# Kernel tuning notes

Hardware: AMD Instinct MI355X
Metric: run time of the kernel (lower is better)

The kernel has to match this reference:

```python
import jax, jax.numpy as jnp
import numpy as np

B, S, D = 2, 2048, 2048
H, HKV, HD = 16, 2, 128
THETA = 10000.0


def setup_inputs() -> dict:
    key = jax.random.key(0)
    ks = jax.random.split(key, 5)
    x = jax.random.normal(ks[0], (B, S, D), jnp.float32)
    Wq = jax.random.normal(ks[1], (D, H * HD), jnp.float32) * 0.02
    Wk = jax.random.normal(ks[2], (D, HKV * HD), jnp.float32) * 0.02
    Wv = jax.random.normal(ks[3], (D, HKV * HD), jnp.float32) * 0.02
    Wo = jax.random.normal(ks[4], (H * HD, D), jnp.float32) * 0.02
    mask = jnp.tril(jnp.ones((S, S), jnp.int32))[None, None]  # causal [1,1,S,S]
    return {"x": x, "mask": mask, "Wq": Wq, "Wk": Wk, "Wv": Wv, "Wo": Wo}


def _rope(t, seq_len):
    # t: [B, S, H, HD]; matches RotaryPositionalEmbedding (cos/sin broadcast [S,1,HD])
    inv_freq = 1.0 / (THETA ** (jnp.arange(0, HD, 2, dtype=jnp.float32) / HD))
    pos = jnp.arange(seq_len, dtype=jnp.float32)
    freqs = jnp.einsum('i,j->ij', pos, inv_freq)          # [S, HD/2]
    emb = jnp.concatenate([freqs, freqs], axis=-1)        # [S, HD]
    cos = jnp.cos(emb)[:, None, :]
    sin = jnp.sin(emb)[:, None, :]
    x1, x2 = jnp.split(t, 2, axis=-1)
    rot = jnp.concatenate([-x2, x1], axis=-1)             # rotate_half
    return t * cos + rot * sin


def reference(x, mask, Wq, Wk, Wv, Wo):
    Bx, Sx, _ = x.shape
    q = (x @ Wq).reshape(Bx, Sx, H, HD)
    k = (x @ Wk).reshape(Bx, Sx, HKV, HD)
    v = (x @ Wv).reshape(Bx, Sx, HKV, HD)
    q = _rope(q, Sx)
    k = _rope(k, Sx)
    rep = H // HKV
    # torch .repeat along head dim == tiling (not interleaved)
    k = jnp.tile(k, (1, 1, rep, 1))  # [B, S, H, HD]
    v = jnp.tile(v, (1, 1, rep, 1))
    scale = 1.0 / np.sqrt(HD).astype(np.float32)
    scores = jnp.einsum('bqhd,bkhd->bhqk', q, k) * scale  # [B, H, S, S]
    scores = jnp.where(mask == 0, -jnp.inf, scores)
    attn = jax.nn.softmax(scores.astype(jnp.float32), axis=-1).astype(scores.dtype)
    out = jnp.einsum('bhqk,bkhd->bqhd', attn, v).reshape(Bx, Sx, H * HD)
    return out @ Wo
```

## Files before the change

### kernel.cpp

```cpp
#include <hip/hip_runtime.h>
#include <hip/hip_bf16.h>

#define S_LEN 2048
#define DMODEL 2048
#define NHEAD 16
#define NKVH 2
#define HDIM 128
#define NROW 4096
#define NQKV 2560
#define SCALE 0.08838834764831845f
#define LOG2E 1.4426950408889634f

using short8 = __attribute__((ext_vector_type(8))) short;
using bf16x8 = __attribute__((ext_vector_type(8))) __bf16;
using f32x4  = __attribute__((ext_vector_type(4))) float;

__device__ __forceinline__ f32x4 mfma16(short8 a, short8 b, f32x4 c) {
  return __builtin_amdgcn_mfma_f32_16x16x32_bf16(
      __builtin_bit_cast(bf16x8, a), __builtin_bit_cast(bf16x8, b), c, 0, 0, 0);
}

__device__ __forceinline__ void gload_lds16(const void* g, void* l) {
  __builtin_amdgcn_global_load_lds(
      (const __attribute__((address_space(1))) unsigned int*)g,
      (__attribute__((address_space(3))) unsigned int*)l, 16, 0, 0);
}

__device__ __forceinline__ float fast_exp2(float x) {
  return __builtin_amdgcn_exp2f(x);
}

__device__ __forceinline__ void storeC(float* C, long idx, float v) { C[idx] = v; }
__device__ __forceinline__ void storeC(__hip_bfloat16* C, long idx, float v) {
  C[idx] = __float2bfloat16(v);
}

__device__ __forceinline__ unsigned short bf16bits(float f) {
  __hip_bfloat16 h = __float2bfloat16(f);
  return *(unsigned short*)&h;
}

__global__ void prep_kernel(const float* __restrict__ x, __hip_bfloat16* __restrict__ xb,
                            const float* __restrict__ Wq, const float* __restrict__ Wk,
                            const float* __restrict__ Wv, __hip_bfloat16* __restrict__ wt1,
                            const float* __restrict__ Wo, __hip_bfloat16* __restrict__ wto,
                            float* __restrict__ cost, float* __restrict__ sint) {
  __shared__ float t[32][33];
  const int bid = blockIdx.x;
  const int tid = threadIdx.x;
  if (bid < 8192) {
    long i = ((long)bid * 256 + tid) * 4;
    float4 v = *(const float4*)(x + i);
    __hip_bfloat16 o[4];
    o[0] = __float2bfloat16(v.x); o[1] = __float2bfloat16(v.y);
    o[2] = __float2bfloat16(v.z); o[3] = __float2bfloat16(v.w);
    *(ushort4*)(xb + i) = *(const ushort4*)o;
  } else if (bid < 17408) {
    int tx = tid & 31, ty = tid >> 5;
    const float* src; int Ns, n0, row_off, kt;
    __hip_bfloat16* dst;
    if (bid < 13312) {
      int r = bid - 8192;
      int nt = r % 80; kt = r / 80;
      dst = wt1;
      if (nt < 64)      { src = Wq; Ns = 2048; n0 = nt * 32;        row_off = n0; }
      else if (nt < 72) { src = Wk; Ns = 256;  n0 = (nt - 64) * 32; row_off = 2048 + n0; }
      else              { src = Wv; Ns = 256;  n0 = (nt - 72) * 32; row_off = 2304 + n0; }
    } else {
      int r = bid - 13312;
      int nt = r % 64; kt = r / 64;
      src = Wo; Ns = 2048; n0 = nt * 32; row_off = n0;
      dst = wto;
    }
#pragma unroll
    for (int i = 0; i < 4; i++)
      t[ty + i * 8][tx] = src[(long)(kt * 32 + ty + i * 8) * Ns + n0 + tx];
    __syncthreads();
#pragma unroll
    for (int i = 0; i < 4; i++)
      dst[(long)(row_off + ty + i * 8) * 2048 + kt * 32 + tx] =
          __float2bfloat16(t[tx][ty + i * 8]);
  } else {
    int i = (bid - 17408) * 256 + tid;
    int s = i >> 6, j = i & 63;
    float f = powf(10000.0f, -(float)j / 64.0f);
    float a = (float)s * f;
    cost[i] = cosf(a);
    sint[i] = sinf(a);
  }
}

template <typename OutT>
__global__ void gemm_bt(const __hip_bfloat16* __restrict__ A,
                        const __hip_bfloat16* __restrict__ Bt,
                        OutT* __restrict__ C, int M, int N, int K) {
  __shared__ __align__(16) __hip_bfloat16 a_lds[2][128 * 32];
  __shared__ __align__(16) __hip_bfloat16 b_lds[2][128 * 32];
  const int tid = threadIdx.x;
  const int wid = tid >> 6, lane = tid & 63;
  const int nbx = gridDim.x;
  int bid = blockIdx.y * nbx + blockIdx.x;
  const int nwg = nbx * gridDim.y;
  bid = (bid & 7) * (nwg >> 3) + (bid >> 3);
  const int m0 = (bid / nbx) * 128, n0 = (bid % nbx) * 128;
  const int wr = wid >> 1, wc = wid & 1;
  const int lrow = lane & 15, lk = lane >> 4;

  const __hip_bfloat16* ag0 = A + (long)(m0 + wid * 16 + (lane >> 2)) * K + (lane & 3) * 8;
  const __hip_bfloat16* bg0 = Bt + (long)(n0 + wid * 16 + (lane >> 2)) * K + (lane & 3) * 8;
  char* al0 = (char*)&a_lds[0][0] + wid * 1024 + lane * 16;
  char* al1 = (char*)&a_lds[1][0] + wid * 1024 + lane * 16;
  char* bl0 = (char*)&b_lds[0][0] + wid * 1024 + lane * 16;
  char* bl1 = (char*)&b_lds[1][0] + wid * 1024 + lane * 16;

  f32x4 acc[4][4] = {};

  for (int k0 = 0; k0 < K; k0 += 64) {
    gload_lds16(ag0 + k0, al0);
    gload_lds16(ag0 + 64 * (long)K + k0, al0 + 4096);
    gload_lds16(ag0 + k0 + 32, al1);
    gload_lds16(ag0 + 64 * (long)K + k0 + 32, al1 + 4096);
    gload_lds16(bg0 + k0, bl0);
    gload_lds16(bg0 + 64 * (long)K + k0, bl0 + 4096);
    gload_lds16(bg0 + k0 + 32, bl1);
    gload_lds16(bg0 + 64 * (long)K + k0 + 32, bl1 + 4096);
    __syncthreads();
#pragma unroll
    for (int hh = 0; hh < 2; hh++) {
      short8 af[4], bfr[4];
#pragma unroll
      for (int mi = 0; mi < 4; mi++)
        af[mi] = *(const short8*)(&a_lds[hh][0] + (wr * 64 + mi * 16 + lrow) * 32 + lk * 8);
#pragma unroll
      for (int ni = 0; ni < 4; ni++)
        bfr[ni] = *(const short8*)(&b_lds[hh][0] + (wc * 64 + ni * 16 + lrow) * 32 + lk * 8);
#pragma unroll
      for (int mi = 0; mi < 4; mi++)
#pragma unroll
        for (int ni = 0; ni < 4; ni++)
          acc[mi][ni] = mfma16(af[mi], bfr[ni], acc[mi][ni]);
    }
    __syncthreads();
  }
#pragma unroll
  for (int mi = 0; mi < 4; mi++)
#pragma unroll
    for (int ni = 0; ni < 4; ni++)
#pragma unroll
      for (int r = 0; r < 4; r++) {
        long row = m0 + wr * 64 + mi * 16 + lk * 4 + r;
        long col = n0 + wc * 64 + ni * 16 + lrow;
        storeC(C, row * N + col, acc[mi][ni][r]);
      }
}

__global__ void rope_vtrans(const __hip_bfloat16* __restrict__ qkv,
                            const float* __restrict__ cost, const float* __restrict__ sint,
                            __hip_bfloat16* __restrict__ q_r, __hip_bfloat16* __restrict__ k_t,
                            __hip_bfloat16* __restrict__ v_t) {
  __shared__ __hip_bfloat16 t[32][33];
  const int bid = blockIdx.x;
  const int tid = threadIdx.x;
  if (bid < 18432) {
    long row = (long)bid * 4 + (tid >> 6);
    int j = tid & 63;
    int hh = (int)(row % 18);
    long bs = row / 18;
    int s = (int)(bs & (S_LEN - 1));
    int b = (int)(bs >> 11);
    const __hip_bfloat16* src = qkv + bs * NQKV;
    float c = cost[s * 64 + j], sn = sint[s * 64 + j];
    if (hh < NHEAD) {
      int col0 = hh * HDIM;
      float lo = __bfloat162float(src[col0 + j]);
      float hi = __bfloat162float(src[col0 + j + 64]);
      __hip_bfloat16* dst = q_r + ((long)(b * NHEAD + hh) * S_LEN + s) * HDIM;
      const float qs = SCALE * LOG2E;
      dst[j]      = __float2bfloat16((lo * c - hi * sn) * qs);
      dst[j + 64] = __float2bfloat16((hi * c + lo * sn) * qs);
    } else {
      int kvh = hh - NHEAD;
      int col0 = DMODEL + kvh * HDIM;
      float lo = __bfloat162float(src[col0 + j]);
      float hi = __bfloat162float(src[col0 + j + 64]);
      long tb = (long)(b * NKVH + kvh) * (S_LEN * HDIM) + (long)(s >> 5) * 4096 +
                (s & 15) * 8 + (j & 7);
      int cs4 = ((s >> 4) & 1) * 4;
      int lkq = ((j >> 3) & 3) * 16;
      int dch = j >> 5;
      k_t[tb + (long)((cs4 + dch) * 64 + lkq) * 8]     = __float2bfloat16(lo * c - hi * sn);
      k_t[tb + (long)((cs4 + dch + 2) * 64 + lkq) * 8] = __float2bfloat16(hi * c + lo * sn);
    }
  } else {
    int r = bid - 18432;
    int st = r & 63, dt = (r >> 6) & 3, bk = r >> 8;
    int tx = tid & 31, ty = tid >> 5;
#pragma unroll
    for (int i = 0; i < 4; i++)
      t[ty + i * 8][tx] = qkv[((long)(bk >> 1) * S_LEN + st * 32 + ty + i * 8) * NQKV +
                              DMODEL + NKVH * HDIM + (bk & 1) * HDIM + dt * 32 + tx];
    __syncthreads();
    long base = (long)bk * (S_LEN * HDIM) + (long)st * 4096 + (tx >> 3) * 128 + (tx & 7);
#pragma unroll
    for (int i = 0; i < 4; i++) {
      int d = dt * 32 + ty + i * 8;
      v_t[base + (long)((d >> 4) * 64 + (d & 15)) * 8] = t[tx][ty + i * 8];
    }
  }
}

__global__ __launch_bounds__(512, 2) void attn_kernel(
    const __hip_bfloat16* __restrict__ q_r, const __hip_bfloat16* __restrict__ k_t,
    const __hip_bfloat16* __restrict__ v_t, __hip_bfloat16* __restrict__ attn_a) {
  __shared__ __align__(16) __hip_bfloat16 k_st[2][4096];
  __shared__ __align__(16) __hip_bfloat16 v_st[2][4096];
  __shared__ __align__(16) __hip_bfloat16 p_lds[8][2 * 16 * 40];
  const int tid = threadIdx.x;
  const int wid = tid >> 6, lane = tid & 63;
  const int lrow = lane & 15, lk = lane >> 4;
  const int bidx = blockIdx.x;
  const int pr = bidx & 31;
  const int hg = (bidx >> 5) & 1;
  const int kv = (bidx >> 6) & 1;
  const int b = bidx >> 7;
  const int myc = (wid < 4) ? pr : (63 - pr);
  const int h = kv + 2 * (hg * 4 + (wid & 3));
  const int q0 = myc * 32;
  const int nkt_w = myc + 1;
  const int NV = 64 - pr;

  const __hip_bfloat16* qb = q_r + (long)(b * NHEAD + h) * S_LEN * HDIM;
  const __hip_bfloat16* kbase = k_t + (long)(b * NKVH + kv) * (S_LEN * HDIM);
  const __hip_bfloat16* vbase = v_t + (long)(b * NKVH + kv) * (S_LEN * HDIM);

  char* kd0 = (char*)&k_st[0][0] + tid * 16;
  char* kd1 = (char*)&k_st[1][0] + tid * 16;
  char* vd0 = (char*)&v_st[0][0] + tid * 16;
  char* vd1 = (char*)&v_st[1][0] + tid * 16;

  short8 qf[2][4];
#pragma unroll
  for (int m = 0; m < 2; m++)
#pragma unroll
    for (int dc = 0; dc < 4; dc++)
      qf[m][dc] = *(const short8*)(qb + (long)(q0 + m * 16 + lrow) * HDIM + dc * 32 + lk * 8);

  f32x4 oacc[2][8] = {};
  float mrow[2] = {5.77f, 5.77f};
  float lsum[2] = {0.f, 0.f};

  gload_lds16(kbase + tid * 8, kd0);
  gload_lds16(vbase + tid * 8, vd0);
  __syncthreads();

  for (int kt = 0; kt < NV; kt++) {
    const char* ks = (const char*)&k_st[kt & 1][0];
    const char* vs = (const char*)&v_st[kt & 1][0];
    if (kt + 1 < NV) {
      gload_lds16(kbase + (long)(kt + 1) * 4096 + tid * 8, (kt & 1) ? kd0 : kd1);
      gload_lds16(vbase + (long)(kt + 1) * 4096 + tid * 8, (kt & 1) ? vd0 : vd1);
    }
    if (kt < nkt_w) {
      const int kc0 = kt * 32;
      short8 kf[2][4];
#pragma unroll
      for (int cs = 0; cs < 2; cs++)
#pragma unroll
        for (int dc = 0; dc < 4; dc++)
          kf[cs][dc] = *(const short8*)(ks + ((cs * 4 + dc) * 64 + lane) * 16);
      short8 vf[8];
#pragma unroll
      for (int d2 = 0; d2 < 8; d2++)
        vf[d2] = *(const short8*)(vs + (d2 * 64 + lane) * 16);
      f32x4 sacc[2][2] = {};
#pragma unroll
      for (int dc = 0; dc < 4; dc++) {
        sacc[0][0] = mfma16(kf[0][dc], qf[0][dc], sacc[0][0]);
        sacc[0][1] = mfma16(kf[1][dc], qf[0][dc], sacc[0][1]);
        sacc[1][0] = mfma16(kf[0][dc], qf[1][dc], sacc[1][0]);
        sacc[1][1] = mfma16(kf[1][dc], qf[1][dc], sacc[1][1]);
      }
      const bool diag = (kt == nkt_w - 1);
#pragma unroll
      for (int m = 0; m < 2; m++) {
        float pv[8];
#pragma unroll
        for (int cs = 0; cs < 2; cs++)
#pragma unroll
          for (int r = 0; r < 4; r++) pv[cs * 4 + r] = sacc[m][cs][r];
        if (diag) {
          int qrow = q0 + m * 16 + lrow;
#pragma unroll
          for (int cs = 0; cs < 2; cs++)
#pragma unroll
            for (int r = 0; r < 4; r++)
              if (kc0 + cs * 16 + lk * 4 + r > qrow) pv[cs * 4 + r] = -3.0e38f;
        }
        float mx = fmaxf(fmaxf(fmaxf(pv[0], pv[1]), fmaxf(pv[2], pv[3])),
                         fmaxf(fmaxf(pv[4], pv[5]), fmaxf(pv[6], pv[7])));
        if (__builtin_expect(__any(mx > mrow[m] + 11.55f), 0)) {
          float mr = fmaxf(mx, __shfl_xor(mx, 16));
          mr = fmaxf(mr, __shfl_xor(mr, 32));
          float mnew = fmaxf(mrow[m], mr);
          float fr = fast_exp2(mrow[m] - mnew);
          lsum[m] *= fr;
          mrow[m] = mnew;
#pragma unroll
          for (int r2 = 0; r2 < 4; r2++) {
            float fro = __shfl(fr, lk * 4 + r2);
#pragma unroll
            for (int d2 = 0; d2 < 8; d2++) oacc[m][d2][r2] *= fro;
          }
        }
        float pe[8];
#pragma unroll
        for (int i = 0; i < 8; i++) pe[i] = fast_exp2(pv[i] - mrow[m]);
        lsum[m] += ((pe[0] + pe[1]) + (pe[2] + pe[3])) + ((pe[4] + pe[5]) + (pe[6] + pe[7]));
        unsigned short pk[8];
#pragma unroll
        for (int i = 0; i < 8; i++) pk[i] = bf16bits(pe[i]);
        *(ushort4*)(&p_lds[wid][(m * 16 + lrow) * 40 + lk * 4]) = *(ushort4*)&pk[0];
        *(ushort4*)(&p_lds[wid][(m * 16 + lrow) * 40 + 16 + lk * 4]) = *(ushort4*)&pk[4];
      }
      short8 pf[2];
#pragma unroll
      for (int m = 0; m < 2; m++)
        pf[m] = *(const short8*)(&p_lds[wid][(m * 16 + lrow) * 40 + lk * 8]);
#pragma unroll
      for (int d2 = 0; d2 < 8; d2++) {
        oacc[0][d2] = mfma16(pf[0], vf[d2], oacc[0][d2]);
        oacc[1][d2] = mfma16(pf[1], vf[d2], oacc[1][d2]);
      }
    }
    __syncthreads();
  }

#pragma unroll
  for (int m = 0; m < 2; m++) {
    float ls = lsum[m];
    ls += __shfl_xor(ls, 16);
    ls += __shfl_xor(ls, 32);
    float inv = 1.0f / ls;
#pragma unroll
    for (int r = 0; r < 4; r++) {
      float invr = __shfl(inv, lk * 4 + r);
      long row = (long)b * S_LEN + q0 + m * 16 + lk * 4 + r;
#pragma unroll
      for (int d2 = 0; d2 < 8; d2++)
        attn_a[row * DMODEL + h * HDIM + d2 * 16 + lrow] =
            __float2bfloat16(oacc[m][d2][r] * invr);
    }
  }
}

extern "C" void kernel_launch(void* const* d_in, const int* in_sizes, int n_in,
                              void* d_out, int out_size, void* d_ws, size_t ws_size,
                              hipStream_t stream) {
  const float* x  = (const float*)d_in[0];
  const float* Wq = (const float*)d_in[2];
  const float* Wk = (const float*)d_in[3];
  const float* Wv = (const float*)d_in[4];
  const float* Wo = (const float*)d_in[5];
  float* out = (float*)d_out;

  char* ws = (char*)d_ws;
  __hip_bfloat16* xb     = (__hip_bfloat16*)(ws + 0);
  __hip_bfloat16* attn_a = xb;
  __hip_bfloat16* wt1    = (__hip_bfloat16*)(ws + 16777216);
  __hip_bfloat16* wto    = (__hip_bfloat16*)(ws + 27262976);
  __hip_bfloat16* qkv    = (__hip_bfloat16*)(ws + 35651584);
  __hip_bfloat16* q_r    = (__hip_bfloat16*)(ws + 56623104);
  __hip_bfloat16* k_t    = (__hip_bfloat16*)(ws + 73400320);
  __hip_bfloat16* v_t    = (__hip_bfloat16*)(ws + 75497472);
  float* cost            = (float*)(ws + 77594624);
  float* sint            = (float*)(ws + 78118912);

  prep_kernel<<<17920, 256, 0, stream>>>(x, xb, Wq, Wk, Wv, wt1, Wo, wto, cost, sint);

  gemm_bt<__hip_bfloat16><<<dim3(20, 32), 256, 0, stream>>>(xb, wt1, qkv, NROW, NQKV, DMODEL);

  rope_vtrans<<<19456, 256, 0, stream>>>(qkv, cost, sint, q_r, k_t, v_t);

  attn_kernel<<<256, 512, 0, stream>>>(q_r, k_t, v_t, attn_a);

  gemm_bt<float><<<dim3(16, 32), 256, 0, stream>>>(attn_a, wto, out, NROW, DMODEL, DMODEL);
}
```

Measured before the change: 182.1 us.

## Fuse RoPE and K/V layout transforms into QKV GEMM epilogue

Replaces the separate QKV GEMM plus rope_vtrans kernel with a single GEMM whose epilogue stages the output tile in LDS, then applies RoPE with scaling for Q and K and writes the swizzled K/V layouts directly. This removes one kernel launch and the global write and re-read of the intermediate qkv buffer. In exchange the epilogue becomes heavier and uses extra LDS, and the work per tile becomes uneven between Q, K and V tiles.

```diff
diff --git a/kernel.cpp b/kernel.cpp
--- a/kernel.cpp
+++ b/kernel.cpp
@@ -38,6 +38,11 @@
 __device__ __forceinline__ unsigned short bf16bits(float f) {
   __hip_bfloat16 h = __float2bfloat16(f);
   return *(unsigned short*)&h;
+}
+
+__device__ __forceinline__ float bf2f(unsigned short u) {
+  unsigned int x = ((unsigned int)u) << 16;
+  return *(float*)&x;
 }
 
 __global__ void prep_kernel(const float* __restrict__ x, __hip_bfloat16* __restrict__ xb,
@@ -154,57 +159,127 @@
       }
 }
 
-__global__ void rope_vtrans(const __hip_bfloat16* __restrict__ qkv,
-                            const float* __restrict__ cost, const float* __restrict__ sint,
-                            __hip_bfloat16* __restrict__ q_r, __hip_bfloat16* __restrict__ k_t,
-                            __hip_bfloat16* __restrict__ v_t) {
-  __shared__ __hip_bfloat16 t[32][33];
-  const int bid = blockIdx.x;
+__global__ __launch_bounds__(256) void gemm_qkv(
+    const __hip_bfloat16* __restrict__ A, const __hip_bfloat16* __restrict__ Bt,
+    const float* __restrict__ cost, const float* __restrict__ sint,
+    __hip_bfloat16* __restrict__ q_r, __hip_bfloat16* __restrict__ k_t,
+    __hip_bfloat16* __restrict__ v_t) {
+  __shared__ __align__(16) char smem[33792];
+  __hip_bfloat16* c_lds = (__hip_bfloat16*)smem;
+  const int K = DMODEL;
   const int tid = threadIdx.x;
-  if (bid < 18432) {
-    long row = (long)bid * 4 + (tid >> 6);
-    int j = tid & 63;
-    int hh = (int)(row % 18);
-    long bs = row / 18;
-    int s = (int)(bs & (S_LEN - 1));
-    int b = (int)(bs >> 11);
-    const __hip_bfloat16* src = qkv + bs * NQKV;
-    float c = cost[s * 64 + j], sn = sint[s * 64 + j];
-    if (hh < NHEAD) {
-      int col0 = hh * HDIM;
-      float lo = __bfloat162float(src[col0 + j]);
-      float hi = __bfloat162float(src[col0 + j + 64]);
-      __hip_bfloat16* dst = q_r + ((long)(b * NHEAD + hh) * S_LEN + s) * HDIM;
-      const float qs = SCALE * LOG2E;
-      dst[j]      = __float2bfloat16((lo * c - hi * sn) * qs);
-      dst[j + 64] = __float2bfloat16((hi * c + lo * sn) * qs);
-    } else {
-      int kvh = hh - NHEAD;
-      int col0 = DMODEL + kvh * HDIM;
-      float lo = __bfloat162float(src[col0 + j]);
-      float hi = __bfloat162float(src[col0 + j + 64]);
-      long tb = (long)(b * NKVH + kvh) * (S_LEN * HDIM) + (long)(s >> 5) * 4096 +
-                (s & 15) * 8 + (j & 7);
-      int cs4 = ((s >> 4) & 1) * 4;
-      int lkq = ((j >> 3) & 3) * 16;
-      int dch = j >> 5;
-      k_t[tb + (long)((cs4 + dch) * 64 + lkq) * 8]     = __float2bfloat16(lo * c - hi * sn);
-      k_t[tb + (long)((cs4 + dch + 2) * 64 + lkq) * 8] = __float2bfloat16(hi * c + lo * sn);
+  const int wid = tid >> 6, lane = tid & 63;
+  const int nbx = gridDim.x;
+  int bid = blockIdx.y * nbx + blockIdx.x;
+  const int nwg = nbx * gridDim.y;
+  bid = (bid & 7) * (nwg >> 3) + (bid >> 3);
+  const int m0 = (bid / nbx) * 128, n0 = (bid % nbx) * 128;
+  const int nt = bid % nbx;
+  const int wr = wid >> 1, wc = wid & 1;
+  const int lrow = lane & 15, lk = lane >> 4;
+
+  const __hip_bfloat16* ag0 = A + (long)(m0 + wid * 16 + (lane >> 2)) * K + (lane & 3) * 8;
+  const __hip_bfloat16* bg0 = Bt + (long)(n0 + wid * 16 + (lane >> 2)) * K + (lane & 3) * 8;
+  char* al0 = smem + wid * 1024 + lane * 16;
+  char* al1 = smem + 8192 + wid * 1024 + lane * 16;
+  char* bl0 = smem + 16384 + wid * 1024 + lane * 16;
+  char* bl1 = smem + 24576 + wid * 1024 + lane * 16;
+
+  f32x4 acc[4][4] = {};
+
+  for (int k0 = 0; k0 < K; k0 += 64) {
+    gload_lds16(ag0 + k0, al0);
+    gload_lds16(ag0 + 64 * (long)K + k0, al0 + 4096);
+    gload_lds16(ag0 + k0 + 32, al1);
+    gload_lds16(ag0 + 64 * (long)K + k0 + 32, al1 + 4096);
+    gload_lds16(bg0 + k0, bl0);
+    gload_lds16(bg0 + 64 * (long)K + k0, bl0 + 4096);
+    gload_lds16(bg0 + k0 + 32, bl1);
+    gload_lds16(bg0 + 64 * (long)K + k0 + 32, bl1 + 4096);
+    __syncthreads();
+#pragma unroll
+    for (int hh = 0; hh < 2; hh++) {
+      const __hip_bfloat16* ab = (const __hip_bfloat16*)(smem + hh * 8192);
+      const __hip_bfloat16* bb = (const __hip_bfloat16*)(smem + 16384 + hh * 8192);
+      short8 af[4], bfr[4];
+#pragma unroll
+      for (int mi = 0; mi < 4; mi++)
+        af[mi] = *(const short8*)(ab + (wr * 64 + mi * 16 + lrow) * 32 + lk * 8);
+#pragma unroll
+      for (int ni = 0; ni < 4; ni++)
+        bfr[ni] = *(const short8*)(bb + (wc * 64 + ni * 16 + lrow) * 32 + lk * 8);
+#pragma unroll
+      for (int mi = 0; mi < 4; mi++)
+#pragma unroll
+        for (int ni = 0; ni < 4; ni++)
+          acc[mi][ni] = mfma16(af[mi], bfr[ni], acc[mi][ni]);
+    }
+    __syncthreads();
+  }
+
+#pragma unroll
+  for (int mi = 0; mi < 4; mi++)
+#pragma unroll
+    for (int ni = 0; ni < 4; ni++)
+#pragma unroll
+      for (int r = 0; r < 4; r++)
+        c_lds[(wr * 64 + mi * 16 + lk * 4 + r) * 132 + wc * 64 + ni * 16 + lrow] =
+            __float2bfloat16(acc[mi][ni][r]);
+  __syncthreads();
+
+  const int b = m0 >> 11;
+  const int s0 = m0 & (S_LEN - 1);
+  if (nt < 18) {
+    const int row = tid >> 1, half = tid & 1;
+    const int s = s0 + row;
+    const bool isq = nt < 16;
+    __hip_bfloat16* qdst = q_r + ((long)(b * NHEAD + nt) * S_LEN + s) * HDIM;
+    const int kv = nt - 16;
+    __hip_bfloat16* kreg = k_t + (long)(b * NKVH + (kv & 1)) * (S_LEN * HDIM) +
+                           (long)(s >> 5) * 4096 + ((s >> 4) & 1) * 2048 + (s & 15) * 8;
+    const float qs = SCALE * LOG2E;
+#pragma unroll
+    for (int c8 = 0; c8 < 8; c8++) {
+      const int d0 = half * 64 + c8 * 8;
+      const int jj = c8 * 8;
+      short8 v0 = *(const short8*)(c_lds + row * 132 + d0);
+      short8 v1 = *(const short8*)(c_lds + row * 132 + (d0 ^ 64));
+      float4 ca = *(const float4*)(cost + s * 64 + jj);
+      float4 cb = *(const float4*)(cost + s * 64 + jj + 4);
+      float4 sa = *(const float4*)(sint + s * 64 + jj);
+      float4 sb = *(const float4*)(sint + s * 64 + jj + 4);
+      float cc[8] = {ca.x, ca.y, ca.z, ca.w, cb.x, cb.y, cb.z, cb.w};
+      float ss[8] = {sa.x, sa.y, sa.z, sa.w, sb.x, sb.y, sb.z, sb.w};
+      unsigned short o[8];
+#pragma unroll
+      for (int i = 0; i < 8; i++) {
+        float a = bf2f((unsigned short)v0[i]);
+        float p = bf2f((unsigned short)v1[i]);
+        float rr = half ? (a * cc[i] + p * ss[i]) : (a * cc[i] - p * ss[i]);
+        if (isq) rr *= qs;
+        o[i] = bf16bits(rr);
+      }
+      if (isq) {
+        *(short8*)(qdst + d0) = *(short8*)o;
+      } else {
+        *(short8*)(kreg + (d0 >> 5) * 512 + ((d0 >> 3) & 3) * 128) = *(short8*)o;
+      }
     }
   } else {
-    int r = bid - 18432;
-    int st = r & 63, dt = (r >> 6) & 3, bk = r >> 8;
-    int tx = tid & 31, ty = tid >> 5;
-#pragma unroll
-    for (int i = 0; i < 4; i++)
-      t[ty + i * 8][tx] = qkv[((long)(bk >> 1) * S_LEN + st * 32 + ty + i * 8) * NQKV +
-                              DMODEL + NKVH * HDIM + (bk & 1) * HDIM + dt * 32 + tx];
-    __syncthreads();
-    long base = (long)bk * (S_LEN * HDIM) + (long)st * 4096 + (tx >> 3) * 128 + (tx & 7);
-#pragma unroll
-    for (int i = 0; i < 4; i++) {
-      int d = dt * 32 + ty + i * 8;
-      v_t[base + (long)((d >> 4) * 64 + (d & 15)) * 8] = t[tx][ty + i * 8];
+    const int kv = nt - 18;
+    __hip_bfloat16* vreg = v_t + (long)(b * NKVH + kv) * (S_LEN * HDIM);
+    const int d = tid & 127;
+    const int gb = tid >> 7;
+    const long dterm = (long)((d >> 4) * 64 + (d & 15)) * 8;
+#pragma unroll
+    for (int it = 0; it < 8; it++) {
+      const int g = gb + it * 2;
+      const int sg = s0 + g * 8;
+      unsigned short o[8];
+#pragma unroll
+      for (int i = 0; i < 8; i++)
+        o[i] = *(const unsigned short*)(c_lds + (g * 8 + i) * 132 + d);
+      *(short8*)(vreg + (long)(sg >> 5) * 4096 + dterm + (g & 3) * 128) = *(short8*)o;
     }
   }
 }
@@ -368,7 +443,6 @@
   __hip_bfloat16* attn_a = xb;
   __hip_bfloat16* wt1    = (__hip_bfloat16*)(ws + 16777216);
   __hip_bfloat16* wto    = (__hip_bfloat16*)(ws + 27262976);
-  __hip_bfloat16* qkv    = (__hip_bfloat16*)(ws + 35651584);
   __hip_bfloat16* q_r    = (__hip_bfloat16*)(ws + 56623104);
   __hip_bfloat16* k_t    = (__hip_bfloat16*)(ws + 73400320);
   __hip_bfloat16* v_t    = (__hip_bfloat16*)(ws + 75497472);
@@ -377,9 +451,7 @@
 
   prep_kernel<<<17920, 256, 0, stream>>>(x, xb, Wq, Wk, Wv, wt1, Wo, wto, cost, sint);
 
-  gemm_bt<__hip_bfloat16><<<dim3(20, 32), 256, 0, stream>>>(xb, wt1, qkv, NROW, NQKV, DMODEL);
-
-  rope_vtrans<<<19456, 256, 0, stream>>>(qkv, cost, sint, q_r, k_t, v_t);
+  gemm_qkv<<<dim3(20, 32), 256, 0, stream>>>(xb, wt1, cost, sint, q_r, k_t, v_t);
 
   attn_kernel<<<256, 512, 0, stream>>>(q_r, k_t, v_t, attn_a);
 
```

Result: slower. 196.7 us (+8.1%).

## Double-buffer LDS tiles in gemm_bt to prefetch next K-slice during MFMA compute

Applied to the files above, without the earlier changes.

The GEMM kernel now keeps two LDS buffers per operand and issues the async global-to-LDS loads for the next 64-wide K slice before running the MFMAs on the current one. This removes one barrier per iteration and is meant to hide global memory latency behind matrix compute. In exchange, LDS use per workgroup doubles to 64 KB, which can lower the number of resident workgroups per CU.

```diff
diff --git a/kernel.cpp b/kernel.cpp
--- a/kernel.cpp
+++ b/kernel.cpp
@@ -94,8 +94,8 @@
 __global__ void gemm_bt(const __hip_bfloat16* __restrict__ A,
                         const __hip_bfloat16* __restrict__ Bt,
                         OutT* __restrict__ C, int M, int N, int K) {
-  __shared__ __align__(16) __hip_bfloat16 a_lds[2][128 * 32];
-  __shared__ __align__(16) __hip_bfloat16 b_lds[2][128 * 32];
+  __shared__ __align__(16) __hip_bfloat16 a_lds[2][2][128 * 32];
+  __shared__ __align__(16) __hip_bfloat16 b_lds[2][2][128 * 32];
   const int tid = threadIdx.x;
   const int wid = tid >> 6, lane = tid & 63;
   const int nbx = gridDim.x;
@@ -108,32 +108,35 @@
 
   const __hip_bfloat16* ag0 = A + (long)(m0 + wid * 16 + (lane >> 2)) * K + (lane & 3) * 8;
   const __hip_bfloat16* bg0 = Bt + (long)(n0 + wid * 16 + (lane >> 2)) * K + (lane & 3) * 8;
-  char* al0 = (char*)&a_lds[0][0] + wid * 1024 + lane * 16;
-  char* al1 = (char*)&a_lds[1][0] + wid * 1024 + lane * 16;
-  char* bl0 = (char*)&b_lds[0][0] + wid * 1024 + lane * 16;
-  char* bl1 = (char*)&b_lds[1][0] + wid * 1024 + lane * 16;
+  const int off = wid * 1024 + lane * 16;
 
   f32x4 acc[4][4] = {};
 
+  auto stage = [&](int k0, int bi) {
+    gload_lds16(ag0 + k0,                     (char*)&a_lds[bi][0][0] + off);
+    gload_lds16(ag0 + 64 * (long)K + k0,      (char*)&a_lds[bi][0][0] + off + 4096);
+    gload_lds16(ag0 + k0 + 32,                (char*)&a_lds[bi][1][0] + off);
+    gload_lds16(ag0 + 64 * (long)K + k0 + 32, (char*)&a_lds[bi][1][0] + off + 4096);
+    gload_lds16(bg0 + k0,                     (char*)&b_lds[bi][0][0] + off);
+    gload_lds16(bg0 + 64 * (long)K + k0,      (char*)&b_lds[bi][0][0] + off + 4096);
+    gload_lds16(bg0 + k0 + 32,                (char*)&b_lds[bi][1][0] + off);
+    gload_lds16(bg0 + 64 * (long)K + k0 + 32, (char*)&b_lds[bi][1][0] + off + 4096);
+  };
+
+  stage(0, 0);
+  __syncthreads();
+  int bi = 0;
   for (int k0 = 0; k0 < K; k0 += 64) {
-    gload_lds16(ag0 + k0, al0);
-    gload_lds16(ag0 + 64 * (long)K + k0, al0 + 4096);
-    gload_lds16(ag0 + k0 + 32, al1);
-    gload_lds16(ag0 + 64 * (long)K + k0 + 32, al1 + 4096);
-    gload_lds16(bg0 + k0, bl0);
-    gload_lds16(bg0 + 64 * (long)K + k0, bl0 + 4096);
-    gload_lds16(bg0 + k0 + 32, bl1);
-    gload_lds16(bg0 + 64 * (long)K + k0 + 32, bl1 + 4096);
-    __syncthreads();
+    if (k0 + 64 < K) stage(k0 + 64, bi ^ 1);
 #pragma unroll
     for (int hh = 0; hh < 2; hh++) {
       short8 af[4], bfr[4];
 #pragma unroll
       for (int mi = 0; mi < 4; mi++)
-        af[mi] = *(const short8*)(&a_lds[hh][0] + (wr * 64 + mi * 16 + lrow) * 32 + lk * 8);
+        af[mi] = *(const short8*)(&a_lds[bi][hh][0] + (wr * 64 + mi * 16 + lrow) * 32 + lk * 8);
 #pragma unroll
       for (int ni = 0; ni < 4; ni++)
-        bfr[ni] = *(const short8*)(&b_lds[hh][0] + (wc * 64 + ni * 16 + lrow) * 32 + lk * 8);
+        bfr[ni] = *(const short8*)(&b_lds[bi][hh][0] + (wc * 64 + ni * 16 + lrow) * 32 + lk * 8);
 #pragma unroll
       for (int mi = 0; mi < 4; mi++)
 #pragma unroll
@@ -141,6 +144,7 @@
           acc[mi][ni] = mfma16(af[mi], bfr[ni], acc[mi][ni]);
     }
     __syncthreads();
+    bi ^= 1;
   }
 #pragma unroll
   for (int mi = 0; mi < 4; mi++)
```

After: 200.2 us. 9.9% more time.
